# Performance work log

Hardware: AMD Instinct MI355X
Metric: run time of the kernel (lower is better)

The kernel has to match this reference:

```python
import jax, jax.numpy as jnp
import numpy as np

B, N, C = 1, 768, 128


def _safe_cdist(x):
    # Euclidean pairwise distance, grad-safe at zero (diagonal).
    sq = jnp.sum(x * x, axis=-1)  # (b, n)
    d2 = sq[:, :, None] + sq[:, None, :] - 2.0 * jnp.einsum('bmi,bni->bmn', x, x)
    d2 = jnp.maximum(d2, 0.0)
    pos = d2 > 0
    return jnp.where(pos, jnp.sqrt(jnp.where(pos, d2, 1.0)), 0.0)


def _bilinear(h, Wa, ba, Wb, bb):
    # Gated bilinear unit: Linear_a(h) * Linear_b(h)
    return (h @ Wa.T + ba) * (h @ Wb.T + bb)


def setup_inputs() -> dict:
    key = jax.random.key(0)
    ks = jax.random.split(key, 16)
    x = jax.random.normal(ks[0], (B, N, 3), dtype=jnp.float32)

    def lin(k, fan_in, fan_out):
        k1, k2 = jax.random.split(k)
        s = 1.0 / np.sqrt(fan_in)
        W = jax.random.uniform(k1, (fan_out, fan_in), jnp.float32, -s, s)
        b = jax.random.uniform(k2, (fan_out,), jnp.float32, -s, s)
        return W, b

    Wa1, ba1 = lin(ks[1], 3, C)
    Wb1, bb1 = lin(ks[2], 3, C)
    Wa2, ba2 = lin(ks[3], C, C)
    Wb2, bb2 = lin(ks[4], C, C)
    Wa3, ba3 = lin(ks[5], C, C)
    Wb3, bb3 = lin(ks[6], C, C)
    Wf, _ = lin(ks[7], C, 2)  # final bias unused by the einsum in forward
    return {"x": x,
            "Wa1": Wa1, "ba1": ba1, "Wb1": Wb1, "bb1": bb1,
            "Wa2": Wa2, "ba2": ba2, "Wb2": Wb2, "bb2": bb2,
            "Wa3": Wa3, "ba3": ba3, "Wb3": Wb3, "bb3": bb3,
            "Wf": Wf}


def reference(x, Wa1, ba1, Wb1, bb1, Wa2, ba2, Wb2, bb2, Wa3, ba3, Wb3, bb3, Wf):
    b, n, _ = x.shape
    nrm = jnp.linalg.norm(x, axis=-1, keepdims=True)          # (b, n, 1)
    nrm_m = jnp.broadcast_to(nrm, (b, n, n))                  # row norms
    d = _safe_cdist(x)                                        # (b, n, n)
    h = jnp.stack([d, nrm_m, jnp.swapaxes(nrm_m, 1, 2)], axis=-1)  # (b,n,n,3)
    h = _bilinear(h, Wa1, ba1, Wb1, bb1)
    h = _bilinear(h, Wa2, ba2, Wb2, bb2)
    h = _bilinear(h, Wa3, ba3, Wb3, bb3)                      # (b,n,n,C)
    att = jax.nn.softmax(h, axis=-2)                          # softmax over n (dim=-2)
    # einsum('bmnc,bni->bmic') followed by sum over m, fused:
    agg = jnp.einsum('bmnc,bni->bic', att, x)                 # (b, 3, C)
    agg = jnp.swapaxes(agg, 1, 2)                             # (b, C, 3)
    out = jnp.einsum('bnd,on->bod', agg, Wf)                  # (b, 2, 3)
    return jnp.concatenate([x[:, :1], out[:, :2]], axis=1)    # (b, 3, 3)
```

## Files before the change

### kernel.cpp

```cpp
#include <hip/hip_runtime.h>

#define NPTS 768
#define CCH  128
#define NM4  36
#define NM2  10
#define TILE 128
#define NCHUNK 6
#define PAIR (NPTS*CCH)
#define NACC 384
#define FINB 96
#define LOG2E 1.4426950408889634f

typedef float f2 __attribute__((ext_vector_type(2)));

__device__ __forceinline__ float fast_exp2(float x) {
  return __builtin_amdgcn_exp2f(x);
}

__device__ __forceinline__ int t4i(int a, int b, int c) {
  int t = 0;
  for (int aa = 0; aa < a; ++aa) t += (5 - aa) * (6 - aa) / 2;
  for (int bb = 0; bb < b; ++bb) t += (5 - a - bb);
  return t + c;
}
__device__ __forceinline__ int t2i(int a, int b, int c) {
  int t = 0;
  for (int aa = 0; aa < a; ++aa) t += (3 - aa) * (4 - aa) / 2;
  for (int bb = 0; bb < b; ++bb) t += (3 - a - bb);
  return t + c;
}

__global__ __launch_bounds__(128) void k_fold12(
    const float* __restrict__ x,
    const float* __restrict__ Wa1, const float* __restrict__ ba1,
    const float* __restrict__ Wb1, const float* __restrict__ bb1,
    const float* __restrict__ Wa2, const float* __restrict__ ba2,
    const float* __restrict__ Wb2, const float* __restrict__ bb2,
    float* __restrict__ norms, float* __restrict__ C2m,
    float* __restrict__ apart, unsigned int* __restrict__ ticket) {
  __shared__ float sA[128][NM2];
  __shared__ float sB[128][NM2];
  const int c = blockIdx.x;
  const int k = threadIdx.x;

  if (c < 6) {
    const int i = c*128 + k;
    const float p0 = x[3*i], p1 = x[3*i+1], p2 = x[3*i+2];
    norms[i] = sqrtf(p0*p0 + p1*p1 + p2*p2);
  }
  if (c == 6) {
    apart[k] = 0.f; apart[CCH + k] = 0.f; apart[2*CCH + k] = 0.f;
    if (k == 0) *ticket = 0u;
  }

  {
    const float A0 = Wa1[3*k], A1 = Wa1[3*k+1], A2c = Wa1[3*k+2], A3 = ba1[k];
    const float B0 = Wb1[3*k], B1 = Wb1[3*k+1], B2c = Wb1[3*k+2], B3 = bb1[k];
    const float g0 = A3*B3;
    const float g1 = A2c*B3 + A3*B2c;
    const float g2 = A2c*B2c;
    const float g3 = A1*B3 + A3*B1;
    const float g4 = A1*B2c + A2c*B1;
    const float g5 = A1*B1;
    const float g6 = A0*B3 + A3*B0;
    const float g7 = A0*B2c + A2c*B0;
    const float g8 = A0*B1 + A1*B0;
    const float g9 = A0*B0;
    const float wa = Wa2[c*CCH + k];
    const float wb = Wb2[c*CCH + k];
    sA[k][0] = wa*g0; sB[k][0] = wb*g0;
    sA[k][1] = wa*g1; sB[k][1] = wb*g1;
    sA[k][2] = wa*g2; sB[k][2] = wb*g2;
    sA[k][3] = wa*g3; sB[k][3] = wb*g3;
    sA[k][4] = wa*g4; sB[k][4] = wb*g4;
    sA[k][5] = wa*g5; sB[k][5] = wb*g5;
    sA[k][6] = wa*g6; sB[k][6] = wb*g6;
    sA[k][7] = wa*g7; sB[k][7] = wb*g7;
    sA[k][8] = wa*g8; sB[k][8] = wb*g8;
    sA[k][9] = wa*g9; sB[k][9] = wb*g9;
  }
  __syncthreads();

  for (int s = 64; s >= 1; s >>= 1) {
    if (k < s) {
      for (int t = 0; t < NM2; ++t) {
        sA[k][t] += sA[k+s][t];
        sB[k][t] += sB[k+s][t];
      }
    }
    __syncthreads();
  }
  if (k == 0) {
    sA[0][0] += ba2[c];
    sB[0][0] += bb2[c];
  }
  __syncthreads();

  if (k < 35) {
    int rem = k, a = 0;
    while (rem >= (5 - a)*(6 - a)/2) { rem -= (5 - a)*(6 - a)/2; ++a; }
    int b = 0;
    while (rem >= 5 - a - b) { rem -= 5 - a - b; ++b; }
    const int cc = rem;
    float s = 0.f;
    const int deg = a + b + cc;
    for (int a1 = 0; a1 <= a && a1 <= 2; ++a1)
      for (int b1 = 0; b1 <= b && b1 <= 2; ++b1)
        for (int c1 = 0; c1 <= cc && c1 <= 2; ++c1) {
          const int d1 = a1 + b1 + c1;
          if (d1 <= 2 && (deg - d1) <= 2)
            s += sA[0][t2i(a1, b1, c1)]
               * sB[0][t2i(a - a1, b - b1, cc - c1)];
        }
    C2m[c*NM4 + k] = s;
  }
  if (k == 35) C2m[c*NM4 + 35] = 0.f;
}

__global__ void k_pre2(const float* __restrict__ Wa3, const float* __restrict__ ba3,
                       const float* __restrict__ Wb3, const float* __restrict__ bb3,
                       const float* __restrict__ C2m,
                       float* __restrict__ A3mT, float* __restrict__ B3mT) {
  const int c = blockIdx.x;
  const int j = threadIdx.x;
  if (j >= NM4) return;
  float sa = 0.f, sb = 0.f;
  if (j < 35) {
    for (int k = 0; k < CCH; ++k) {
      const float v = C2m[k*NM4 + j];
      sa += Wa3[c*CCH + k] * v;
      sb += Wb3[c*CCH + k] * v;
    }
    if (j == 0) { sa += ba3[c]; sb += bb3[c]; }
  }
  A3mT[j*CCH + c] = sa;
  B3mT[j*CCH + c] = sb;
}

__global__ __launch_bounds__(256) void k_main(
    const float* __restrict__ x, const float* __restrict__ norms,
    const float* __restrict__ A3mT, const float* __restrict__ B3mT,
    float* __restrict__ Mp, float* __restrict__ Sp,
    float* __restrict__ A0p, float* __restrict__ A1p, float* __restrict__ A2p) {
  __shared__ f2 wdv[2][TILE];
  __shared__ __align__(16) float4 xt[TILE];
  const int tid = threadIdx.x;
  const int mi = tid >> 7;
  const int c = tid & 127;
  const int m = blockIdx.x*2 + mi;
  const int chunk = blockIdx.y;

  const float u = norms[m];
  const float xm0 = x[3*m], xm1 = x[3*m+1], xm2 = x[3*m+2];

  {
    const int n = chunk*TILE + c;
    const float v = norms[n];
    const float x0 = x[3*n], x1 = x[3*n+1], x2 = x[3*n+2];
    const float dot = xm0*x0 + xm1*x1 + xm2*x2;
    const float d2 = u*u + v*v - 2.f*dot;
    const float d = (d2 > 0.f) ? sqrtf(d2) : 0.f;
    f2 dv; dv.x = d; dv.y = v;
    wdv[mi][c] = dv;
    if (mi == 0) xt[c] = make_float4(x0, x1, x2, 1.0f);
  }

  float upow[5]; upow[0] = 1.f;
  #pragma unroll
  for (int b = 1; b < 5; ++b) upow[b] = upow[b-1]*u;
  float cA[15], cB[15];
  {
    int t = 0;
    #pragma unroll
    for (int i = 0; i <= 4; ++i)
      #pragma unroll
      for (int j = 0; i + j <= 4; ++j) {
        float sa = 0.f, sb = 0.f;
        #pragma unroll
        for (int b = 0; i + j + b <= 4; ++b) {
          const int t4 = t4i(i, b, j);
          sa += A3mT[t4*CCH + c]*upow[b];
          sb += B3mT[t4*CCH + c]*upow[b];
        }
        cA[t] = sa*LOG2E; cB[t] = sb; ++t;
      }
  }

  __syncthreads();

  float mrun = -INFINITY, srun = 0.f, a0 = 0.f, a1 = 0.f, a2 = 0.f;
  for (int base = 0; base < TILE; base += 8) {
    float h[8];
    #pragma unroll
    for (int q = 0; q < 8; ++q) {
      const f2 dv = wdv[mi][base + q];
      const float d = dv.x;
      const float v = dv.y;
      float pa = fmaf(fmaf(fmaf(fmaf(cA[4], v, cA[3]), v, cA[2]), v, cA[1]), v, cA[0]);
      float qa = fmaf(fmaf(fmaf(cA[8], v, cA[7]), v, cA[6]), v, cA[5]);
      float ra = fmaf(fmaf(cA[11], v, cA[10]), v, cA[9]);
      float sa = fmaf(cA[13], v, cA[12]);
      const float la = fmaf(fmaf(fmaf(fmaf(cA[14], d, sa), d, ra), d, qa), d, pa);
      float pb = fmaf(fmaf(fmaf(fmaf(cB[4], v, cB[3]), v, cB[2]), v, cB[1]), v, cB[0]);
      float qb = fmaf(fmaf(fmaf(cB[8], v, cB[7]), v, cB[6]), v, cB[5]);
      float rb = fmaf(fmaf(cB[11], v, cB[10]), v, cB[9]);
      float sb = fmaf(cB[13], v, cB[12]);
      const float lb = fmaf(fmaf(fmaf(fmaf(cB[14], d, sb), d, rb), d, qb), d, pb);
      h[q] = la * lb;
    }
    const float m01 = fmaxf(h[0], h[1]), m23 = fmaxf(h[2], h[3]);
    const float m45 = fmaxf(h[4], h[5]), m67 = fmaxf(h[6], h[7]);
    const float m8 = fmaxf(fmaxf(m01, m23), fmaxf(m45, m67));
    const float mnew = fmaxf(mrun, m8);
    const float scale = fast_exp2(mrun - mnew);
    srun *= scale; a0 *= scale; a1 *= scale; a2 *= scale;
    #pragma unroll
    for (int q = 0; q < 8; ++q) {
      const float e = fast_exp2(h[q] - mnew);
      const float4 vx = xt[base + q];
      srun += e;
      a0 = fmaf(e, vx.x, a0);
      a1 = fmaf(e, vx.y, a1);
      a2 = fmaf(e, vx.z, a2);
    }
    mrun = mnew;
  }
  const int idx = chunk*PAIR + m*CCH + c;
  Mp[idx] = mrun; Sp[idx] = srun;
  A0p[idx] = a0; A1p[idx] = a1; A2p[idx] = a2;
}

__global__ __launch_bounds__(256) void k_fin(
    const float* __restrict__ x,
    const float* __restrict__ Mp, const float* __restrict__ Sp,
    const float* __restrict__ A0p, const float* __restrict__ A1p,
    const float* __restrict__ A2p,
    const float* __restrict__ Wf,
    float* __restrict__ apart, unsigned int* __restrict__ ticket,
    float* __restrict__ out) {
  __shared__ float red2[2][3][CCH];
  __shared__ float red[CCH][6];
  __shared__ bool last;
  const int tid = threadIdx.x;
  const int ml = tid >> 7;
  const int c = tid & 127;

  float s0 = 0.f, s1 = 0.f, s2 = 0.f;
  #pragma unroll
  for (int j = 0; j < 4; ++j) {
    const int m = blockIdx.x*8 + ml*4 + j;
    const int gid = m*CCH + c;
    float m0 = Mp[0*PAIR + gid], m1 = Mp[1*PAIR + gid], m2 = Mp[2*PAIR + gid];
    float m3 = Mp[3*PAIR + gid], m4 = Mp[4*PAIR + gid], m5 = Mp[5*PAIR + gid];
    float M = fmaxf(fmaxf(fmaxf(m0, m1), fmaxf(m2, m3)), fmaxf(m4, m5));
    float W = 0.f, g0 = 0.f, g1 = 0.f, g2 = 0.f;
    {
      const float e0 = fast_exp2(m0 - M), e1 = fast_exp2(m1 - M);
      const float e2 = fast_exp2(m2 - M), e3 = fast_exp2(m3 - M);
      const float e4 = fast_exp2(m4 - M), e5 = fast_exp2(m5 - M);
      W = Sp[0*PAIR+gid]*e0 + Sp[1*PAIR+gid]*e1 + Sp[2*PAIR+gid]*e2
        + Sp[3*PAIR+gid]*e3 + Sp[4*PAIR+gid]*e4 + Sp[5*PAIR+gid]*e5;
      g0 = A0p[0*PAIR+gid]*e0 + A0p[1*PAIR+gid]*e1 + A0p[2*PAIR+gid]*e2
         + A0p[3*PAIR+gid]*e3 + A0p[4*PAIR+gid]*e4 + A0p[5*PAIR+gid]*e5;
      g1 = A1p[0*PAIR+gid]*e0 + A1p[1*PAIR+gid]*e1 + A1p[2*PAIR+gid]*e2
         + A1p[3*PAIR+gid]*e3 + A1p[4*PAIR+gid]*e4 + A1p[5*PAIR+gid]*e5;
      g2 = A2p[0*PAIR+gid]*e0 + A2p[1*PAIR+gid]*e1 + A2p[2*PAIR+gid]*e2
         + A2p[3*PAIR+gid]*e3 + A2p[4*PAIR+gid]*e4 + A2p[5*PAIR+gid]*e5;
    }
    const float inv = 1.f / W;
    s0 = fmaf(g0, inv, s0);
    s1 = fmaf(g1, inv, s1);
    s2 = fmaf(g2, inv, s2);
  }
  red2[ml][0][c] = s0; red2[ml][1][c] = s1; red2[ml][2][c] = s2;
  __syncthreads();
  for (int p = tid; p < NACC; p += 256) {
    const int i = p >> 7, cc = p & 127;
    atomicAdd(&apart[p], red2[0][i][cc] + red2[1][i][cc]);
  }
  __threadfence();
  __syncthreads();
  if (tid == 0) {
    const unsigned int old = atomicAdd(ticket, 1u);
    last = (old == FINB - 1);
  }
  __syncthreads();
  if (!last) return;
  __threadfence();

  if (tid < CCH) {
    const int cc = tid;
    const float a0 = __hip_atomic_load(&apart[cc],          __ATOMIC_RELAXED, __HIP_MEMORY_SCOPE_AGENT);
    const float a1 = __hip_atomic_load(&apart[CCH + cc],    __ATOMIC_RELAXED, __HIP_MEMORY_SCOPE_AGENT);
    const float a2 = __hip_atomic_load(&apart[2*CCH + cc],  __ATOMIC_RELAXED, __HIP_MEMORY_SCOPE_AGENT);
    const float w0 = Wf[cc], w1 = Wf[CCH + cc];
    red[cc][0] = w0*a0; red[cc][1] = w0*a1; red[cc][2] = w0*a2;
    red[cc][3] = w1*a0; red[cc][4] = w1*a1; red[cc][5] = w1*a2;
  }
  __syncthreads();
  if (tid < 6) {
    float s = 0.f;
    for (int k = 0; k < CCH; ++k) s += red[k][tid];
    out[3 + tid] = s;
  }
  if (tid < 3) out[tid] = x[tid];
}

extern "C" void kernel_launch(void* const* d_in, const int* in_sizes, int n_in,
                              void* d_out, int out_size, void* d_ws, size_t ws_size,
                              hipStream_t stream) {
  const float* x   = (const float*)d_in[0];
  const float* Wa1 = (const float*)d_in[1];
  const float* ba1 = (const float*)d_in[2];
  const float* Wb1 = (const float*)d_in[3];
  const float* bb1 = (const float*)d_in[4];
  const float* Wa2 = (const float*)d_in[5];
  const float* ba2 = (const float*)d_in[6];
  const float* Wb2 = (const float*)d_in[7];
  const float* bb2 = (const float*)d_in[8];
  const float* Wa3 = (const float*)d_in[9];
  const float* ba3 = (const float*)d_in[10];
  const float* Wb3 = (const float*)d_in[11];
  const float* bb3 = (const float*)d_in[12];
  const float* Wf  = (const float*)d_in[13];
  float* out = (float*)d_out;

  float* ws     = (float*)d_ws;
  float* norms  = ws;
  float* C2m    = norms + NPTS;
  float* A3mT   = C2m   + CCH*NM4;
  float* B3mT   = A3mT  + NM4*CCH;
  float* Mp     = B3mT  + NM4*CCH;
  float* Sp     = Mp    + NCHUNK*PAIR;
  float* A0p    = Sp    + NCHUNK*PAIR;
  float* A1p    = A0p   + NCHUNK*PAIR;
  float* A2p    = A1p   + NCHUNK*PAIR;
  float* apart  = A2p   + NCHUNK*PAIR;
  unsigned int* ticket = (unsigned int*)(apart + NACC);

  hipLaunchKernelGGL(k_fold12, dim3(CCH), dim3(128), 0, stream,
                     x, Wa1, ba1, Wb1, bb1, Wa2, ba2, Wb2, bb2,
                     norms, C2m, apart, ticket);
  hipLaunchKernelGGL(k_pre2, dim3(CCH), dim3(64), 0, stream,
                     Wa3, ba3, Wb3, bb3, C2m, A3mT, B3mT);
  hipLaunchKernelGGL(k_main, dim3(NPTS/2, NCHUNK), dim3(256), 0, stream,
                     x, norms, A3mT, B3mT, Mp, Sp, A0p, A1p, A2p);
  hipLaunchKernelGGL(k_fin, dim3(FINB), dim3(256), 0, stream,
                     x, Mp, Sp, A0p, A1p, A2p, Wf, apart, ticket, out);
}
```

Before: 169.5 us.

## Evaluate per-pair polynomial via split-bf16 MFMA instead of scalar Horner FMAs

Moves the per-(m,n,c) bivariate degree-4 polynomial evaluation onto MFMA 32x32x16 bf16 instructions. Each fp32 value is split into three bf16 pieces and six MFMA products are accumulated to recover near-fp32 accuracy. A new pre-kernel precomputes the per-row coefficients in split-bf16 packed form, and k_main now assigns one wave per row m with two half-waves merging softmax partials. The aim is to cut VALU FMA cost, at the price of a new kernel, extra global traffic for the coefficient tables, and possible precision loss.

Result: no change. 172.2 us (+1.6%).

```diff
diff --git a/kernel.cpp b/kernel.cpp
--- a/kernel.cpp
+++ b/kernel.cpp
@@ -10,11 +10,25 @@
 #define NACC 384
 #define FINB 96
 #define LOG2E 1.4426950408889634f
-
-typedef float f2 __attribute__((ext_vector_type(2)));
+#define NQW  (NPTS*8*CCH)
+
+typedef __attribute__((ext_vector_type(8))) short bf16x8;
+typedef __attribute__((ext_vector_type(16))) float f32x16;
+union Frag { unsigned int u[4]; bf16x8 h; };
 
 __device__ __forceinline__ float fast_exp2(float x) {
   return __builtin_amdgcn_exp2f(x);
+}
+
+__device__ __forceinline__ void split3(float x, unsigned int& h0,
+                                       unsigned int& h1, unsigned int& h2) {
+  const unsigned int b0 = __float_as_uint(x);
+  h0 = b0 >> 16;
+  const float r1 = x - __uint_as_float(b0 & 0xFFFF0000u);
+  const unsigned int b1 = __float_as_uint(r1);
+  h1 = b1 >> 16;
+  const float r2 = r1 - __uint_as_float(b1 & 0xFFFF0000u);
+  h2 = __float_as_uint(r2) >> 16;
 }
 
 __device__ __forceinline__ int t4i(int a, int b, int c) {
@@ -137,97 +151,186 @@
   B3mT[j*CCH + c] = sb;
 }
 
-__global__ __launch_bounds__(256) void k_main(
+__global__ __launch_bounds__(256) void k_pre3(
+    const float* __restrict__ norms,
+    const float* __restrict__ A3mT, const float* __restrict__ B3mT,
+    unsigned int* __restrict__ WA0, unsigned int* __restrict__ WA1,
+    unsigned int* __restrict__ WA2, unsigned int* __restrict__ WB0,
+    unsigned int* __restrict__ WB1, unsigned int* __restrict__ WB2) {
+  const int m = blockIdx.x;
+  const float u = norms[m];
+  float upow[5];
+  upow[0] = 1.f; upow[1] = u; upow[2] = u*u;
+  upow[3] = upow[2]*u; upow[4] = upow[2]*upow[2];
+
+  for (int p = threadIdx.x; p < 8*CCH; p += 256) {
+    const int q = p >> 7;
+    const int c = p & 127;
+    unsigned int wa0 = 0, wa1 = 0, wa2 = 0, wb0 = 0, wb1 = 0, wb2 = 0;
+    #pragma unroll
+    for (int half = 0; half < 2; ++half) {
+      const int t = 2*q + half;
+      int rem = t, i = 0;
+      while (i < 5 && rem >= 5 - i) { rem -= 5 - i; ++i; }
+      const int j = rem;
+      float sa = 0.f, sb = 0.f;
+      #pragma unroll
+      for (int b = 0; b < 5; ++b) {
+        if (i <= 4 && i + j + b <= 4) {
+          const int idx = t4i(i, b, j)*CCH + c;
+          sa = fmaf(A3mT[idx], upow[b], sa);
+          sb = fmaf(B3mT[idx], upow[b], sb);
+        }
+      }
+      sa *= LOG2E;
+      unsigned int a0, a1, a2, b0, b1, b2;
+      split3(sa, a0, a1, a2);
+      split3(sb, b0, b1, b2);
+      const int sh = half*16;
+      wa0 |= a0 << sh; wa1 |= a1 << sh; wa2 |= a2 << sh;
+      wb0 |= b0 << sh; wb1 |= b1 << sh; wb2 |= b2 << sh;
+    }
+    const int o = (m*8 + q)*CCH + c;
+    WA0[o] = wa0; WA1[o] = wa1; WA2[o] = wa2;
+    WB0[o] = wb0; WB1[o] = wb1; WB2[o] = wb2;
+  }
+}
+
+__global__ __launch_bounds__(256, 2) void k_main(
     const float* __restrict__ x, const float* __restrict__ norms,
-    const float* __restrict__ A3mT, const float* __restrict__ B3mT,
+    const unsigned int* __restrict__ WA0, const unsigned int* __restrict__ WA1,
+    const unsigned int* __restrict__ WA2, const unsigned int* __restrict__ WB0,
+    const unsigned int* __restrict__ WB1, const unsigned int* __restrict__ WB2,
     float* __restrict__ Mp, float* __restrict__ Sp,
     float* __restrict__ A0p, float* __restrict__ A1p, float* __restrict__ A2p) {
-  __shared__ f2 wdv[2][TILE];
   __shared__ __align__(16) float4 xt[TILE];
   const int tid = threadIdx.x;
-  const int mi = tid >> 7;
-  const int c = tid & 127;
-  const int m = blockIdx.x*2 + mi;
+  const int wid = tid >> 6;
+  const int lane = tid & 63;
+  const int hl = lane >> 5;
+  const int ln = lane & 31;
+  const int m = blockIdx.x*4 + wid;
   const int chunk = blockIdx.y;
+
+  if (tid < TILE) {
+    const int n = chunk*TILE + tid;
+    xt[tid] = make_float4(x[3*n], x[3*n+1], x[3*n+2], norms[n]);
+  }
 
   const float u = norms[m];
   const float xm0 = x[3*m], xm1 = x[3*m+1], xm2 = x[3*m+2];
-
-  {
-    const int n = chunk*TILE + c;
-    const float v = norms[n];
-    const float x0 = x[3*n], x1 = x[3*n+1], x2 = x[3*n+2];
-    const float dot = xm0*x0 + xm1*x1 + xm2*x2;
-    const float d2 = u*u + v*v - 2.f*dot;
+  const float uu = u*u;
+
+  Frag BA0[4], BA1[4], BA2[4], BB0[4], BB1[4], BB2[4];
+  #pragma unroll
+  for (int ct = 0; ct < 4; ++ct) {
+    #pragma unroll
+    for (int p = 0; p < 4; ++p) {
+      const int o = (m*8 + hl*4 + p)*CCH + ct*32 + ln;
+      BA0[ct].u[p] = WA0[o]; BA1[ct].u[p] = WA1[o]; BA2[ct].u[p] = WA2[o];
+      BB0[ct].u[p] = WB0[o]; BB1[ct].u[p] = WB1[o]; BB2[ct].u[p] = WB2[o];
+    }
+  }
+
+  float mrun[4], srun[4], a0r[4], a1r[4], a2r[4];
+  #pragma unroll
+  for (int ct = 0; ct < 4; ++ct) {
+    mrun[ct] = -INFINITY; srun[ct] = 0.f;
+    a0r[ct] = 0.f; a1r[ct] = 0.f; a2r[ct] = 0.f;
+  }
+
+  __syncthreads();
+
+  for (int tile = 0; tile < 4; ++tile) {
+    const float4 xn = xt[tile*32 + ln];
+    const float v = xn.w;
+    const float dot = xm0*xn.x + xm1*xn.y + xm2*xn.z;
+    const float d2 = uu + v*v - 2.f*dot;
     const float d = (d2 > 0.f) ? sqrtf(d2) : 0.f;
-    f2 dv; dv.x = d; dv.y = v;
-    wdv[mi][c] = dv;
-    if (mi == 0) xt[c] = make_float4(x0, x1, x2, 1.0f);
-  }
-
-  float upow[5]; upow[0] = 1.f;
+    const float v2 = v*v, v3 = v2*v, v4 = v2*v2;
+    const float dd = d*d, d3 = dd*d, d4 = dd*dd;
+    float mono[8];
+    if (hl == 0) {
+      mono[0] = 1.f;   mono[1] = v;     mono[2] = v2;    mono[3] = v3;
+      mono[4] = v4;    mono[5] = d;     mono[6] = d*v;   mono[7] = d*v2;
+    } else {
+      mono[0] = d*v3;  mono[1] = dd;    mono[2] = dd*v;  mono[3] = dd*v2;
+      mono[4] = d3;    mono[5] = d3*v;  mono[6] = d4;    mono[7] = 0.f;
+    }
+    Frag A0f, A1f, A2f;
+    #pragma unroll
+    for (int p = 0; p < 4; ++p) {
+      unsigned int l0, l1, l2, g0, g1, g2;
+      split3(mono[2*p],   l0, l1, l2);
+      split3(mono[2*p+1], g0, g1, g2);
+      A0f.u[p] = l0 | (g0 << 16);
+      A1f.u[p] = l1 | (g1 << 16);
+      A2f.u[p] = l2 | (g2 << 16);
+    }
+
+    #pragma unroll
+    for (int ct = 0; ct < 4; ++ct) {
+      f32x16 accA, accB;
+      #pragma unroll
+      for (int r = 0; r < 16; ++r) { accA[r] = 0.f; accB[r] = 0.f; }
+      accA = __builtin_amdgcn_mfma_f32_32x32x16_bf16(A2f.h, BA0[ct].h, accA, 0, 0, 0);
+      accA = __builtin_amdgcn_mfma_f32_32x32x16_bf16(A1f.h, BA1[ct].h, accA, 0, 0, 0);
+      accA = __builtin_amdgcn_mfma_f32_32x32x16_bf16(A0f.h, BA2[ct].h, accA, 0, 0, 0);
+      accA = __builtin_amdgcn_mfma_f32_32x32x16_bf16(A1f.h, BA0[ct].h, accA, 0, 0, 0);
+      accA = __builtin_amdgcn_mfma_f32_32x32x16_bf16(A0f.h, BA1[ct].h, accA, 0, 0, 0);
+      accA = __builtin_amdgcn_mfma_f32_32x32x16_bf16(A0f.h, BA0[ct].h, accA, 0, 0, 0);
+      accB = __builtin_amdgcn_mfma_f32_32x32x16_bf16(A2f.h, BB0[ct].h, accB, 0, 0, 0);
+      accB = __builtin_amdgcn_mfma_f32_32x32x16_bf16(A1f.h, BB1[ct].h, accB, 0, 0, 0);
+      accB = __builtin_amdgcn_mfma_f32_32x32x16_bf16(A0f.h, BB2[ct].h, accB, 0, 0, 0);
+      accB = __builtin_amdgcn_mfma_f32_32x32x16_bf16(A1f.h, BB0[ct].h, accB, 0, 0, 0);
+      accB = __builtin_amdgcn_mfma_f32_32x32x16_bf16(A0f.h, BB1[ct].h, accB, 0, 0, 0);
+      accB = __builtin_amdgcn_mfma_f32_32x32x16_bf16(A0f.h, BB0[ct].h, accB, 0, 0, 0);
+
+      float hv[16];
+      #pragma unroll
+      for (int r = 0; r < 16; ++r) hv[r] = accA[r]*accB[r];
+      float hx = hv[0];
+      #pragma unroll
+      for (int r = 1; r < 16; ++r) hx = fmaxf(hx, hv[r]);
+      const float mnew = fmaxf(mrun[ct], hx);
+      const float sc = fast_exp2(mrun[ct] - mnew);
+      mrun[ct] = mnew;
+      float s_ = srun[ct]*sc, A0_ = a0r[ct]*sc, A1_ = a1r[ct]*sc, A2_ = a2r[ct]*sc;
+      #pragma unroll
+      for (int rg = 0; rg < 4; ++rg) {
+        #pragma unroll
+        for (int q = 0; q < 4; ++q) {
+          const float e = fast_exp2(hv[rg*4 + q] - mnew);
+          const float4 xv = xt[tile*32 + rg*8 + hl*4 + q];
+          s_ += e;
+          A0_ = fmaf(e, xv.x, A0_);
+          A1_ = fmaf(e, xv.y, A1_);
+          A2_ = fmaf(e, xv.z, A2_);
+        }
+      }
+      srun[ct] = s_; a0r[ct] = A0_; a1r[ct] = A1_; a2r[ct] = A2_;
+    }
+  }
+
   #pragma unroll
-  for (int b = 1; b < 5; ++b) upow[b] = upow[b-1]*u;
-  float cA[15], cB[15];
-  {
-    int t = 0;
-    #pragma unroll
-    for (int i = 0; i <= 4; ++i)
-      #pragma unroll
-      for (int j = 0; i + j <= 4; ++j) {
-        float sa = 0.f, sb = 0.f;
-        #pragma unroll
-        for (int b = 0; i + j + b <= 4; ++b) {
-          const int t4 = t4i(i, b, j);
-          sa += A3mT[t4*CCH + c]*upow[b];
-          sb += B3mT[t4*CCH + c]*upow[b];
-        }
-        cA[t] = sa*LOG2E; cB[t] = sb; ++t;
-      }
-  }
-
-  __syncthreads();
-
-  float mrun = -INFINITY, srun = 0.f, a0 = 0.f, a1 = 0.f, a2 = 0.f;
-  for (int base = 0; base < TILE; base += 8) {
-    float h[8];
-    #pragma unroll
-    for (int q = 0; q < 8; ++q) {
-      const f2 dv = wdv[mi][base + q];
-      const float d = dv.x;
-      const float v = dv.y;
-      float pa = fmaf(fmaf(fmaf(fmaf(cA[4], v, cA[3]), v, cA[2]), v, cA[1]), v, cA[0]);
-      float qa = fmaf(fmaf(fmaf(cA[8], v, cA[7]), v, cA[6]), v, cA[5]);
-      float ra = fmaf(fmaf(cA[11], v, cA[10]), v, cA[9]);
-      float sa = fmaf(cA[13], v, cA[12]);
-      const float la = fmaf(fmaf(fmaf(fmaf(cA[14], d, sa), d, ra), d, qa), d, pa);
-      float pb = fmaf(fmaf(fmaf(fmaf(cB[4], v, cB[3]), v, cB[2]), v, cB[1]), v, cB[0]);
-      float qb = fmaf(fmaf(fmaf(cB[8], v, cB[7]), v, cB[6]), v, cB[5]);
-      float rb = fmaf(fmaf(cB[11], v, cB[10]), v, cB[9]);
-      float sb = fmaf(cB[13], v, cB[12]);
-      const float lb = fmaf(fmaf(fmaf(fmaf(cB[14], d, sb), d, rb), d, qb), d, pb);
-      h[q] = la * lb;
-    }
-    const float m01 = fmaxf(h[0], h[1]), m23 = fmaxf(h[2], h[3]);
-    const float m45 = fmaxf(h[4], h[5]), m67 = fmaxf(h[6], h[7]);
-    const float m8 = fmaxf(fmaxf(m01, m23), fmaxf(m45, m67));
-    const float mnew = fmaxf(mrun, m8);
-    const float scale = fast_exp2(mrun - mnew);
-    srun *= scale; a0 *= scale; a1 *= scale; a2 *= scale;
-    #pragma unroll
-    for (int q = 0; q < 8; ++q) {
-      const float e = fast_exp2(h[q] - mnew);
-      const float4 vx = xt[base + q];
-      srun += e;
-      a0 = fmaf(e, vx.x, a0);
-      a1 = fmaf(e, vx.y, a1);
-      a2 = fmaf(e, vx.z, a2);
-    }
-    mrun = mnew;
-  }
-  const int idx = chunk*PAIR + m*CCH + c;
-  Mp[idx] = mrun; Sp[idx] = srun;
-  A0p[idx] = a0; A1p[idx] = a1; A2p[idx] = a2;
+  for (int ct = 0; ct < 4; ++ct) {
+    const float om = __shfl_xor(mrun[ct], 32);
+    const float os = __shfl_xor(srun[ct], 32);
+    const float o0 = __shfl_xor(a0r[ct], 32);
+    const float o1 = __shfl_xor(a1r[ct], 32);
+    const float o2 = __shfl_xor(a2r[ct], 32);
+    const float M  = fmaxf(mrun[ct], om);
+    const float e1 = fast_exp2(mrun[ct] - M);
+    const float e2 = fast_exp2(om - M);
+    if (hl == 0) {
+      const int idx = chunk*PAIR + m*CCH + ct*32 + ln;
+      Mp[idx]  = M;
+      Sp[idx]  = fmaf(srun[ct], e1, os*e2);
+      A0p[idx] = fmaf(a0r[ct], e1, o0*e2);
+      A1p[idx] = fmaf(a1r[ct], e1, o1*e2);
+      A2p[idx] = fmaf(a2r[ct], e1, o2*e2);
+    }
+  }
 }
 
 __global__ __launch_bounds__(256) void k_fin(
@@ -338,13 +441,24 @@
   float* apart  = A2p   + NCHUNK*PAIR;
   unsigned int* ticket = (unsigned int*)(apart + NACC);
 
+  size_t off = (((size_t)((char*)(ticket + 1) - (char*)d_ws)) + 255) & ~(size_t)255;
+  unsigned int* WA0 = (unsigned int*)((char*)d_ws + off);
+  unsigned int* WA1 = WA0 + NQW;
+  unsigned int* WA2 = WA1 + NQW;
+  unsigned int* WB0 = WA2 + NQW;
+  unsigned int* WB1 = WB0 + NQW;
+  unsigned int* WB2 = WB1 + NQW;
+
   hipLaunchKernelGGL(k_fold12, dim3(CCH), dim3(128), 0, stream,
                      x, Wa1, ba1, Wb1, bb1, Wa2, ba2, Wb2, bb2,
                      norms, C2m, apart, ticket);
   hipLaunchKernelGGL(k_pre2, dim3(CCH), dim3(64), 0, stream,
                      Wa3, ba3, Wb3, bb3, C2m, A3mT, B3mT);
-  hipLaunchKernelGGL(k_main, dim3(NPTS/2, NCHUNK), dim3(256), 0, stream,
-                     x, norms, A3mT, B3mT, Mp, Sp, A0p, A1p, A2p);
+  hipLaunchKernelGGL(k_pre3, dim3(NPTS), dim3(256), 0, stream,
+                     norms, A3mT, B3mT, WA0, WA1, WA2, WB0, WB1, WB2);
+  hipLaunchKernelGGL(k_main, dim3(NPTS/4, NCHUNK), dim3(256), 0, stream,
+                     x, norms, WA0, WA1, WA2, WB0, WB1, WB2,
+                     Mp, Sp, A0p, A1p, A2p);
   hipLaunchKernelGGL(k_fin, dim3(FINB), dim3(256), 0, stream,
                      x, Mp, Sp, A0p, A1p, A2p, Wf, apart, ticket, out);
 }
```
